# Kernel optimization log

Measured on AMD Instinct MI355X. Metric: run time of the kernel, lower is better.

The kernel has to match this reference:

```python
import jax, jax.numpy as jnp
import numpy as np

B, C, H, W = 4, 256, 64, 64
CH = C // 2  # inner channels of the non-local block


def _conv1x1(x, w, b):
    # 1x1 conv == channel-mixing einsum; x: [B,C,H,W], w: [O,C], b: [O]
    return jnp.einsum('oc,bchw->bohw', w, x) + b[None, :, None, None]


def setup_inputs() -> dict:
    key = jax.random.key(0)
    ks = jax.random.split(key, 9)
    s = 0.02  # small init so exp(scores) stays in fp32 range (no max-subtraction in this block)
    return {
        'x':  jax.random.normal(ks[0], (B, C, H, W), dtype=jnp.float32),
        'w1': s * jax.random.normal(ks[1], (CH, C), dtype=jnp.float32),
        'b1': jnp.zeros((CH,), jnp.float32),
        'w2': s * jax.random.normal(ks[2], (CH, C), dtype=jnp.float32),
        'b2': jnp.zeros((CH,), jnp.float32),
        'w3': s * jax.random.normal(ks[3], (CH, C), dtype=jnp.float32),
        'b3': jnp.zeros((CH,), jnp.float32),
        'w4': s * jax.random.normal(ks[4], (C, CH), dtype=jnp.float32),
        'b4': jnp.zeros((C,), jnp.float32),
    }


def reference(x, w1, b1, w2, b2, w3, b3, w4, b4):
    b, c, h, w = x.shape
    n = h * w
    theta = _conv1x1(x, w1, b1).reshape(b, -1, n)  # [B, C/2, N]
    phi   = _conv1x1(x, w2, b2).reshape(b, -1, n)  # [B, C/2, N]
    g     = _conv1x1(x, w3, b3).reshape(b, -1, n)  # [B, C/2, N]
    # full non-local affinity: [B, N, N]
    scores = jnp.einsum('bci,bcj->bij', theta, phi)
    attn = jnp.exp(scores)  # faithful: no max-subtraction in the original
    attn = attn / jnp.sum(attn, axis=1, keepdims=True)  # normalize over dim=1 as written
    y = jnp.einsum('bij,bcj->bci', attn, g)  # [B, C/2, N]
    y = y.reshape(b, -1, h, w)               # [B, C/2, H, W]
    out = _conv1x1(y, w4, b4) + x            # project back to C, residual
    return out
```

## Files before the change

kernel.cpp:

```cpp
#include <hip/hip_runtime.h>

#define DEVI __device__ __forceinline__

typedef __attribute__((ext_vector_type(8))) short bf16x8;
typedef __attribute__((ext_vector_type(4))) short bf16x4;
typedef __attribute__((ext_vector_type(4))) float f32x4;

#define MFMA16 __builtin_amdgcn_mfma_f32_16x16x32_bf16

DEVI short f2bs(float f) {
  union { float f; unsigned u; } v; v.f = f;
  unsigned r = v.u + 0x7fffu + ((v.u >> 16) & 1u);
  return (short)(r >> 16);
}
DEVI float bs2f(short s) {
  union { unsigned u; float f; } v; v.u = ((unsigned)(unsigned short)s) << 16;
  return v.f;
}

DEVI void gload_lds16(const short* g, short* lds) {
  __builtin_amdgcn_global_load_lds(
      (const __attribute__((address_space(1))) unsigned int*)g,
      (__attribute__((address_space(3))) unsigned int*)lds, 16, 0, 0);
}

DEVI void stage_chunk(short* lds, const short* g, int ldg, int tid) {
#pragma unroll
  for (int it = 0; it < 2; ++it) {
    int slot = it * 256 + tid;
    int row  = slot >> 2;
    int ko   = (slot & 3) << 3;
    gload_lds16(g + (size_t)row * ldg + ko, lds + slot * 8);
  }
}

DEVI void stage_chunk64(short* lds, const short* g, int ldg, int tid) {
  int row = tid >> 2, ko = (tid & 3) << 3;
  gload_lds16(g + (size_t)row * ldg + ko, lds + tid * 8);
}

DEVI bf16x8 lds8(const short* p) { return *(const bf16x8*)p; }

DEVI void zero_acc(f32x4 (&a)[4][4]) {
  f32x4 z = {0.f, 0.f, 0.f, 0.f};
#pragma unroll
  for (int i = 0; i < 4; ++i)
#pragma unroll
    for (int j = 0; j < 4; ++j) a[i][j] = z;
}

__global__ __launch_bounds__(256) void k_prep(const float* __restrict__ x,
                                              const float* __restrict__ w1,
                                              const float* __restrict__ w2,
                                              const float* __restrict__ w3,
                                              short* __restrict__ xt,
                                              short* __restrict__ w123) {
  int tid = threadIdx.x;
  if (blockIdx.y == 4) {
    int lin = blockIdx.z * 64 + blockIdx.x;
    for (int i = lin * 256 + tid; i < 384 * 256; i += 65536) {
      int r = i >> 8;
      const float* w = (r < 128) ? w1 : (r < 256 ? w2 : w3);
      w123[i] = f2bs(w[(size_t)(r & 127) * 256 + (i & 255)]);
    }
    return;
  }
  __shared__ float t[64][65];
  int b = blockIdx.z;
  int c0 = blockIdx.y * 64;
  int p0 = blockIdx.x * 64;
  const float* xb = x + (size_t)b * 256 * 4096;
#pragma unroll
  for (int i = 0; i < 16; ++i) {
    int idx = i * 256 + tid;
    int c = idx >> 6, p = idx & 63;
    t[p][c] = xb[(size_t)(c0 + c) * 4096 + p0 + p];
  }
  __syncthreads();
  short* xtb = xt + ((size_t)b * 4096 + p0) * 256 + c0;
#pragma unroll
  for (int i = 0; i < 16; ++i) {
    int idx = i * 256 + tid;
    int p = idx >> 6, c = idx & 63;
    xtb[(size_t)p * 256 + c] = f2bs(t[p][c]);
  }
}

__global__ __launch_bounds__(256) void k_proj(const short* __restrict__ xt,
                                              const short* __restrict__ w123,
                                              const float* __restrict__ b1,
                                              const float* __restrict__ b2,
                                              const float* __restrict__ b3,
                                              short* __restrict__ theta,
                                              short* __restrict__ phi,
                                              short* __restrict__ gT) {
  __shared__ short Lp[17408];
  int tid = threadIdx.x;
  int m0 = blockIdx.x * 128;
  int nb = blockIdx.y;
  int b  = blockIdx.z;
  int lane = tid & 63, wid = tid >> 6;
  int col = lane & 15, quad = lane >> 4;
  int wm = (wid >> 1) * 64, wn = (wid & 1) * 64;
  const short* A = xt + ((size_t)b * 4096 + m0) * 256;
  const short* B = w123 + (size_t)nb * 128 * 256;
  short* a0 = Lp;           short* b0 = Lp + 4096;
  short* a1 = Lp + 8192;    short* b1_ = Lp + 12288;
  stage_chunk(a0, A, 256, tid);
  stage_chunk(b0, B, 256, tid);
  f32x4 acc[4][4];
  zero_acc(acc);
  for (int ks = 0; ks < 8; ++ks) {
    short* ac = (ks & 1) ? a1 : a0;
    short* an = (ks & 1) ? a0 : a1;
    short* bc = (ks & 1) ? b1_ : b0;
    short* bn = (ks & 1) ? b0 : b1_;
    __syncthreads();
    if (ks < 7) {
      stage_chunk(an, A + (ks + 1) * 32, 256, tid);
      stage_chunk(bn, B + (ks + 1) * 32, 256, tid);
    }
    bf16x8 af[4], bf_[4];
#pragma unroll
    for (int mi = 0; mi < 4; ++mi) af[mi] = lds8(&ac[(wm + mi * 16 + col) * 32 + quad * 8]);
#pragma unroll
    for (int ni = 0; ni < 4; ++ni) bf_[ni] = lds8(&bc[(wn + ni * 16 + col) * 32 + quad * 8]);
#pragma unroll
    for (int mi = 0; mi < 4; ++mi)
#pragma unroll
      for (int ni = 0; ni < 4; ++ni)
        acc[mi][ni] = MFMA16(af[mi], bf_[ni], acc[mi][ni], 0, 0, 0);
  }
  const float* bias = (nb == 0) ? b1 : (nb == 1 ? b2 : b3);
  __syncthreads();
  short* oL = Lp;
  if (nb < 2) {
#pragma unroll
    for (int mi = 0; mi < 4; ++mi)
#pragma unroll
      for (int ni = 0; ni < 4; ++ni) {
        float bv = bias[wn + ni * 16 + col];
#pragma unroll
        for (int r = 0; r < 4; ++r)
          oL[(wm + mi * 16 + quad * 4 + r) * 136 + wn + ni * 16 + col] = f2bs(acc[mi][ni][r] + bv);
      }
    __syncthreads();
    short* O = ((nb == 0) ? theta : phi) + ((size_t)b * 4096 + m0) * 128;
#pragma unroll
    for (int it = 0; it < 8; ++it) {
      int slot = it * 256 + tid;
      int r = slot >> 4, cp = (slot & 15) * 8;
      *(bf16x8*)(O + (size_t)r * 128 + cp) = lds8(&oL[r * 136 + cp]);
    }
  } else {
#pragma unroll
    for (int mi = 0; mi < 4; ++mi)
#pragma unroll
      for (int ni = 0; ni < 4; ++ni) {
        float bv = bias[wn + ni * 16 + col];
#pragma unroll
        for (int r = 0; r < 4; ++r)
          oL[(wn + ni * 16 + col) * 136 + wm + mi * 16 + quad * 4 + r] = f2bs(acc[mi][ni][r] + bv);
      }
    __syncthreads();
    short* O = gT + (size_t)b * 128 * 4096 + m0;
#pragma unroll
    for (int it = 0; it < 8; ++it) {
      int slot = it * 256 + tid;
      int c = slot >> 4, p8 = (slot & 15) * 8;
      *(bf16x8*)(O + (size_t)c * 4096 + p8) = lds8(&oL[c * 136 + p8]);
    }
  }
}

__global__ __launch_bounds__(256, 2) void k_denom(const short* __restrict__ theta,
                                                  const short* __restrict__ phi,
                                                  float* __restrict__ dpart) {
  __shared__ short L[16384];
  __shared__ float part[128];
  int tid = threadIdx.x;
  int ib = blockIdx.x, jc = blockIdx.y, b = blockIdx.z;
  int lane = tid & 63, wid = tid >> 6;
  int col = lane & 15, quad = lane >> 4;
  int wmj = (wid & 1) * 32;
  int wni = (wid >> 1) * 64;
  const short* TH = theta + ((size_t)b * 4096 + ib * 128) * 128;
  const short* PH = phi + ((size_t)b * 4096 + (size_t)jc * 1024) * 128;
  float* D = dpart + ((size_t)(b * 32 + ib)) * 4096 + jc * 1024;
#pragma unroll
  for (int ks = 0; ks < 4; ++ks) stage_chunk(L + ks * 4096, TH + ks * 32, 128, tid);
  __syncthreads();
  bf16x8 bth[4][4];
#pragma unroll
  for (int ks = 0; ks < 4; ++ks)
#pragma unroll
    for (int ni = 0; ni < 4; ++ni)
      bth[ks][ni] = lds8(&L[ks * 4096 + (wni + ni * 16 + col) * 32 + quad * 8]);
  __syncthreads();
#pragma unroll
  for (int ks = 0; ks < 4; ++ks) stage_chunk64(L + ks * 2048, PH + ks * 32, 128, tid);
  for (int jt = 0; jt < 16; ++jt) {
    short* phc = L + (jt & 1) * 8192;
    short* phn = L + ((jt & 1) ^ 1) * 8192;
    __syncthreads();
    if (jt < 15) {
      const short* PHn = PH + (size_t)(jt + 1) * 64 * 128;
#pragma unroll
      for (int ks = 0; ks < 4; ++ks) stage_chunk64(phn + ks * 2048, PHn + ks * 32, 128, tid);
    }
    f32x4 s[2][4];
#pragma unroll
    for (int mi = 0; mi < 2; ++mi)
#pragma unroll
      for (int ni = 0; ni < 4; ++ni) s[mi][ni] = (f32x4){0.f, 0.f, 0.f, 0.f};
#pragma unroll
    for (int ks = 0; ks < 4; ++ks) {
      bf16x8 ap[2];
#pragma unroll
      for (int mi = 0; mi < 2; ++mi) ap[mi] = lds8(&phc[ks * 2048 + (wmj + mi * 16 + col) * 32 + quad * 8]);
#pragma unroll
      for (int mi = 0; mi < 2; ++mi)
#pragma unroll
        for (int ni = 0; ni < 4; ++ni)
          s[mi][ni] = MFMA16(ap[mi], bth[ks][ni], s[mi][ni], 0, 0, 0);
    }
#pragma unroll
    for (int mi = 0; mi < 2; ++mi)
#pragma unroll
      for (int r = 0; r < 4; ++r) {
        float ps = __expf(s[mi][0][r]) + __expf(s[mi][1][r]) +
                   __expf(s[mi][2][r]) + __expf(s[mi][3][r]);
        ps += __shfl_xor(ps, 1, 16);
        ps += __shfl_xor(ps, 2, 16);
        ps += __shfl_xor(ps, 4, 16);
        ps += __shfl_xor(ps, 8, 16);
        if (col == 0) part[(wid >> 1) * 64 + wmj + mi * 16 + quad * 4 + r] = ps;
      }
    __syncthreads();
    if (tid < 64) D[jt * 64 + tid] = part[tid] + part[64 + tid];
  }
}

__global__ __launch_bounds__(256) void k_dred(const float* __restrict__ dpart,
                                              float* __restrict__ dinv) {
  int b = blockIdx.x >> 2, jb = blockIdx.x & 3;
  int j4 = jb * 1024 + threadIdx.x * 4;
  f32x4 s = {0.f, 0.f, 0.f, 0.f};
  for (int ib = 0; ib < 32; ++ib)
    s += *(const f32x4*)(dpart + ((size_t)(b * 32 + ib)) * 4096 + j4);
  f32x4 r;
#pragma unroll
  for (int e = 0; e < 4; ++e) r[e] = 1.0f / s[e];
  *(f32x4*)(dinv + (size_t)b * 4096 + j4) = r;
}

__global__ __launch_bounds__(256, 2) void k_attn(const short* __restrict__ theta,
                                                 const short* __restrict__ phi,
                                                 const short* __restrict__ gT,
                                                 const float* __restrict__ dinv,
                                                 short* __restrict__ ypart) {
  __shared__ short L[40960];
  int tid = threadIdx.x;
  int ib = blockIdx.x, jc = blockIdx.y, b = blockIdx.z;
  int lane = tid & 63, wid = tid >> 6;
  int col = lane & 15, quad = lane >> 4;
  int wmj = (wid & 1) * 32;
  int wni = (wid >> 1) * 64;
  int wnc = (wid & 1) * 64;
  const short* TH = theta + ((size_t)b * 4096 + ib * 128) * 128;
  const short* PH = phi + ((size_t)b * 4096 + (size_t)jc * 1024) * 128;
  const short* GT = gT + (size_t)b * 128 * 4096 + jc * 1024;
  const float* DI = dinv + (size_t)b * 4096 + jc * 1024;
  short* pP = L + 32768;
#pragma unroll
  for (int ks = 0; ks < 4; ++ks) stage_chunk(L + ks * 4096, TH + ks * 32, 128, tid);
  __syncthreads();
  bf16x8 bth[4][4];
#pragma unroll
  for (int ks = 0; ks < 4; ++ks)
#pragma unroll
    for (int ni = 0; ni < 4; ++ni)
      bth[ks][ni] = lds8(&L[ks * 4096 + (wni + ni * 16 + col) * 32 + quad * 8]);
  __syncthreads();
#pragma unroll
  for (int ks = 0; ks < 4; ++ks) stage_chunk64(L + ks * 2048, PH + ks * 32, 128, tid);
#pragma unroll
  for (int s = 0; s < 2; ++s) stage_chunk(L + 16384 + s * 4096, GT + s * 32, 4096, tid);
  f32x4 accy[4][4];
  zero_acc(accy);
  for (int jt = 0; jt < 16; ++jt) {
    int cur = jt & 1;
    short* phc = L + cur * 8192;
    short* phn = L + (cur ^ 1) * 8192;
    short* gpc = L + 16384 + cur * 8192;
    short* gpn = L + 16384 + (cur ^ 1) * 8192;
    __syncthreads();
    if (jt < 15) {
      const short* PHn = PH + (size_t)(jt + 1) * 64 * 128;
#pragma unroll
      for (int ks = 0; ks < 4; ++ks) stage_chunk64(phn + ks * 2048, PHn + ks * 32, 128, tid);
    }
    f32x4 dv[2];
#pragma unroll
    for (int mi = 0; mi < 2; ++mi)
      dv[mi] = *(const f32x4*)(DI + jt * 64 + wmj + mi * 16 + quad * 4);
    f32x4 s[2][4];
#pragma unroll
    for (int mi = 0; mi < 2; ++mi)
#pragma unroll
      for (int ni = 0; ni < 4; ++ni) s[mi][ni] = (f32x4){0.f, 0.f, 0.f, 0.f};
#pragma unroll
    for (int ks = 0; ks < 4; ++ks) {
      bf16x8 ap[2];
#pragma unroll
      for (int mi = 0; mi < 2; ++mi) ap[mi] = lds8(&phc[ks * 2048 + (wmj + mi * 16 + col) * 32 + quad * 8]);
#pragma unroll
      for (int mi = 0; mi < 2; ++mi)
#pragma unroll
        for (int ni = 0; ni < 4; ++ni)
          s[mi][ni] = MFMA16(ap[mi], bth[ks][ni], s[mi][ni], 0, 0, 0);
    }
#pragma unroll
    for (int mi = 0; mi < 2; ++mi) {
      int j0 = wmj + mi * 16 + quad * 4;
      int blk = j0 >> 3, off = j0 & 7;
#pragma unroll
      for (int ni = 0; ni < 4; ++ni) {
        int i = wni + ni * 16 + col;
        bf16x4 pv;
#pragma unroll
        for (int r = 0; r < 4; ++r) pv[r] = f2bs(__expf(s[mi][ni][r]) * dv[mi][r]);
        *(bf16x4*)(pP + i * 64 + ((blk ^ (i & 7)) << 3) + off) = pv;
      }
    }
    __syncthreads();
    if (jt < 15) {
      const short* GTn = GT + (jt + 1) * 64;
#pragma unroll
      for (int s2 = 0; s2 < 2; ++s2) stage_chunk(gpn + s2 * 4096, GTn + s2 * 32, 4096, tid);
    }
#pragma unroll
    for (int ksj = 0; ksj < 2; ++ksj) {
      bf16x8 ap2[4], bg[4];
#pragma unroll
      for (int mi = 0; mi < 4; ++mi) {
        int i = wni + mi * 16 + col;
        ap2[mi] = lds8(&pP[i * 64 + (((ksj * 4 + quad) ^ (i & 7)) << 3)]);
      }
#pragma unroll
      for (int ni = 0; ni < 4; ++ni) bg[ni] = lds8(&gpc[ksj * 4096 + (wnc + ni * 16 + col) * 32 + quad * 8]);
#pragma unroll
      for (int mi = 0; mi < 4; ++mi)
#pragma unroll
        for (int ni = 0; ni < 4; ++ni)
          accy[mi][ni] = MFMA16(ap2[mi], bg[ni], accy[mi][ni], 0, 0, 0);
    }
  }
  short* Yp = ypart + ((size_t)(jc * 4 + b) * 4096 + (size_t)ib * 128) * 128;
#pragma unroll
  for (int half = 0; half < 2; ++half) {
    __syncthreads();
    if ((wid >> 1) == half) {
#pragma unroll
      for (int mi = 0; mi < 4; ++mi)
#pragma unroll
        for (int ni = 0; ni < 4; ++ni)
#pragma unroll
          for (int r = 0; r < 4; ++r)
            pP[(mi * 16 + quad * 4 + r) * 128 + wnc + ni * 16 + col] = f2bs(accy[mi][ni][r]);
    }
    __syncthreads();
#pragma unroll
    for (int it = 0; it < 4; ++it) {
      int slot = it * 256 + tid;
      int r = slot >> 4, c8 = (slot & 15) * 8;
      *(bf16x8*)(Yp + (size_t)(half * 64 + r) * 128 + c8) = lds8(&pP[r * 128 + c8]);
    }
  }
}

__global__ __launch_bounds__(256) void k_out(const short* __restrict__ ypart,
                                             const float* __restrict__ w4,
                                             const float* __restrict__ b4,
                                             const float* __restrict__ x,
                                             float* __restrict__ out) {
  __shared__ short wL[4 * 4096];
  __shared__ short yL[4 * 4096];
  __shared__ float bLs[128];
  int tid = threadIdx.x;
  int ibk = blockIdx.x, ob = blockIdx.y, b = blockIdx.z;
  int o0 = ob * 128, i0 = ibk * 128;
  int lane = tid & 63, wid = tid >> 6;
  int col = lane & 15, quad = lane >> 4;
  int wm = (wid >> 1) * 64, wn = (wid & 1) * 64;
#pragma unroll
  for (int it = 0; it < 16; ++it) {
    int slot = it * 256 + tid;
    int r = slot >> 5, c4 = (slot & 31) * 4;
    int ks = c4 >> 5, cr = c4 & 31;
    f32x4 wv = *(const f32x4*)(w4 + (size_t)(o0 + r) * 128 + c4);
    bf16x4 wp;
#pragma unroll
    for (int e = 0; e < 4; ++e) wp[e] = f2bs(wv[e]);
    *(bf16x4*)&wL[ks * 4096 + r * 32 + cr] = wp;
  }
#pragma unroll
  for (int it = 0; it < 8; ++it) {
    int slot = it * 256 + tid;
    int r = slot >> 4, c8 = (slot & 15) * 8;
    int ks = c8 >> 5, cr = c8 & 31;
    float a8[8];
#pragma unroll
    for (int e = 0; e < 8; ++e) a8[e] = 0.f;
#pragma unroll
    for (int p = 0; p < 4; ++p) {
      bf16x8 v = *(const bf16x8*)(ypart + ((size_t)(p * 4 + b) * 4096 + i0 + r) * 128 + c8);
#pragma unroll
      for (int e = 0; e < 8; ++e) a8[e] += bs2f(v[e]);
    }
    bf16x8 yv;
#pragma unroll
    for (int e = 0; e < 8; ++e) yv[e] = f2bs(a8[e]);
    *(bf16x8*)&yL[ks * 4096 + r * 32 + cr] = yv;
  }
  if (tid < 128) bLs[tid] = b4[o0 + tid];
  __syncthreads();
  f32x4 acc[4][4];
  zero_acc(acc);
#pragma unroll
  for (int ks = 0; ks < 4; ++ks) {
    bf16x8 af[4], bf_[4];
#pragma unroll
    for (int mi = 0; mi < 4; ++mi) af[mi] = lds8(&wL[ks * 4096 + (wm + mi * 16 + col) * 32 + quad * 8]);
#pragma unroll
    for (int ni = 0; ni < 4; ++ni) bf_[ni] = lds8(&yL[ks * 4096 + (wn + ni * 16 + col) * 32 + quad * 8]);
#pragma unroll
    for (int mi = 0; mi < 4; ++mi)
#pragma unroll
      for (int ni = 0; ni < 4; ++ni)
        acc[mi][ni] = MFMA16(af[mi], bf_[ni], acc[mi][ni], 0, 0, 0);
  }
  const float* X = x + ((size_t)b * 256 + o0) * 4096 + i0;
  float* O = out + ((size_t)b * 256 + o0) * 4096 + i0;
#pragma unroll
  for (int mi = 0; mi < 4; ++mi)
#pragma unroll
    for (int ni = 0; ni < 4; ++ni)
#pragma unroll
      for (int r = 0; r < 4; ++r) {
        int o = wm + mi * 16 + quad * 4 + r;
        int i = wn + ni * 16 + col;
        O[(size_t)o * 4096 + i] = acc[mi][ni][r] + X[(size_t)o * 4096 + i] + bLs[o];
      }
}

extern "C" void kernel_launch(void* const* d_in, const int* in_sizes, int n_in,
                              void* d_out, int out_size, void* d_ws, size_t ws_size,
                              hipStream_t stream) {
  const float* x  = (const float*)d_in[0];
  const float* w1 = (const float*)d_in[1];
  const float* b1 = (const float*)d_in[2];
  const float* w2 = (const float*)d_in[3];
  const float* b2 = (const float*)d_in[4];
  const float* w3 = (const float*)d_in[5];
  const float* b3 = (const float*)d_in[6];
  const float* w4 = (const float*)d_in[7];
  const float* b4 = (const float*)d_in[8];
  char* ws = (char*)d_ws;
  short* xt    = (short*)(ws + 0);
  short* w123  = (short*)(ws + 8388608);
  short* theta = (short*)(ws + 8585216);
  short* phi   = (short*)(ws + 12779520);
  short* gT    = (short*)(ws + 16973824);
  float* dpart = (float*)(ws + 21168128);
  float* dinv  = (float*)(ws + 23265280);
  short* ypart = (short*)(ws + 23330816);
  float* out   = (float*)d_out;
  (void)in_sizes; (void)n_in; (void)out_size; (void)ws_size;

  k_prep<<<dim3(64, 5, 4), dim3(256), 0, stream>>>(x, w1, w2, w3, xt, w123);
  k_proj<<<dim3(32, 3, 4), dim3(256), 0, stream>>>(xt, w123, b1, b2, b3, theta, phi, gT);
  k_denom<<<dim3(32, 4, 4), dim3(256), 0, stream>>>(theta, phi, dpart);
  k_dred<<<dim3(16), dim3(256), 0, stream>>>(dpart, dinv);
  k_attn<<<dim3(32, 4, 4), dim3(256), 0, stream>>>(theta, phi, gT, dinv, ypart);
  k_out<<<dim3(32, 2, 4), dim3(256), 0, stream>>>(ypart, w4, b4, x, out);
}
```

Measured before the change: 187.7 us.

## Fuse bf16 prep into projection and merge attention barriers with lgkm waits

Removes the separate transpose/convert kernel. The projection GEMM now reads fp32 x and weights straight from global memory and converts them to bf16 in registers, with no LDS staging. In the attention kernel, the next gT chunk is prefetched together with phi at the top of each tile, which drops one __syncthreads per iteration. The denominator and attention kernels also replace __syncthreads with a waitcnt on LDS only plus s_barrier. The risks are uncoalesced strided global loads of x in the projection (each lane reads 8 values spaced 4096 floats apart) and a possible race, because the barrier no longer waits on outstanding vmcnt for the global-to-LDS loads.

```diff
diff --git a/kernel.cpp b/kernel.cpp
--- a/kernel.cpp
+++ b/kernel.cpp
@@ -16,6 +16,11 @@
 DEVI float bs2f(short s) {
   union { unsigned u; float f; } v; v.u = ((unsigned)(unsigned short)s) << 16;
   return v.f;
+}
+
+DEVI void lgkm_barrier() {
+  __builtin_amdgcn_s_waitcnt(0xC07F);
+  __builtin_amdgcn_s_barrier();
 }
 
 DEVI void gload_lds16(const short* g, short* lds) {
@@ -49,52 +54,17 @@
     for (int j = 0; j < 4; ++j) a[i][j] = z;
 }
 
-__global__ __launch_bounds__(256) void k_prep(const float* __restrict__ x,
-                                              const float* __restrict__ w1,
-                                              const float* __restrict__ w2,
-                                              const float* __restrict__ w3,
-                                              short* __restrict__ xt,
-                                              short* __restrict__ w123) {
-  int tid = threadIdx.x;
-  if (blockIdx.y == 4) {
-    int lin = blockIdx.z * 64 + blockIdx.x;
-    for (int i = lin * 256 + tid; i < 384 * 256; i += 65536) {
-      int r = i >> 8;
-      const float* w = (r < 128) ? w1 : (r < 256 ? w2 : w3);
-      w123[i] = f2bs(w[(size_t)(r & 127) * 256 + (i & 255)]);
-    }
-    return;
-  }
-  __shared__ float t[64][65];
-  int b = blockIdx.z;
-  int c0 = blockIdx.y * 64;
-  int p0 = blockIdx.x * 64;
-  const float* xb = x + (size_t)b * 256 * 4096;
-#pragma unroll
-  for (int i = 0; i < 16; ++i) {
-    int idx = i * 256 + tid;
-    int c = idx >> 6, p = idx & 63;
-    t[p][c] = xb[(size_t)(c0 + c) * 4096 + p0 + p];
-  }
-  __syncthreads();
-  short* xtb = xt + ((size_t)b * 4096 + p0) * 256 + c0;
-#pragma unroll
-  for (int i = 0; i < 16; ++i) {
-    int idx = i * 256 + tid;
-    int p = idx >> 6, c = idx & 63;
-    xtb[(size_t)p * 256 + c] = f2bs(t[p][c]);
-  }
-}
-
-__global__ __launch_bounds__(256) void k_proj(const short* __restrict__ xt,
-                                              const short* __restrict__ w123,
-                                              const float* __restrict__ b1,
-                                              const float* __restrict__ b2,
-                                              const float* __restrict__ b3,
-                                              short* __restrict__ theta,
-                                              short* __restrict__ phi,
-                                              short* __restrict__ gT) {
-  __shared__ short Lp[17408];
+__global__ __launch_bounds__(256, 4) void k_proj(const float* __restrict__ x,
+                                                 const float* __restrict__ w1,
+                                                 const float* __restrict__ w2,
+                                                 const float* __restrict__ w3,
+                                                 const float* __restrict__ b1,
+                                                 const float* __restrict__ b2,
+                                                 const float* __restrict__ b3,
+                                                 short* __restrict__ theta,
+                                                 short* __restrict__ phi,
+                                                 short* __restrict__ gT) {
+  __shared__ short oL[128 * 136];
   int tid = threadIdx.x;
   int m0 = blockIdx.x * 128;
   int nb = blockIdx.y;
@@ -102,29 +72,29 @@
   int lane = tid & 63, wid = tid >> 6;
   int col = lane & 15, quad = lane >> 4;
   int wm = (wid >> 1) * 64, wn = (wid & 1) * 64;
-  const short* A = xt + ((size_t)b * 4096 + m0) * 256;
-  const short* B = w123 + (size_t)nb * 128 * 256;
-  short* a0 = Lp;           short* b0 = Lp + 4096;
-  short* a1 = Lp + 8192;    short* b1_ = Lp + 12288;
-  stage_chunk(a0, A, 256, tid);
-  stage_chunk(b0, B, 256, tid);
+  const float* W = (nb == 0) ? w1 : (nb == 1 ? w2 : w3);
+  const float* X = x + (size_t)b * 256 * 4096;
   f32x4 acc[4][4];
   zero_acc(acc);
+#pragma unroll
   for (int ks = 0; ks < 8; ++ks) {
-    short* ac = (ks & 1) ? a1 : a0;
-    short* an = (ks & 1) ? a0 : a1;
-    short* bc = (ks & 1) ? b1_ : b0;
-    short* bn = (ks & 1) ? b0 : b1_;
-    __syncthreads();
-    if (ks < 7) {
-      stage_chunk(an, A + (ks + 1) * 32, 256, tid);
-      stage_chunk(bn, B + (ks + 1) * 32, 256, tid);
-    }
     bf16x8 af[4], bf_[4];
 #pragma unroll
-    for (int mi = 0; mi < 4; ++mi) af[mi] = lds8(&ac[(wm + mi * 16 + col) * 32 + quad * 8]);
-#pragma unroll
-    for (int ni = 0; ni < 4; ++ni) bf_[ni] = lds8(&bc[(wn + ni * 16 + col) * 32 + quad * 8]);
+    for (int mi = 0; mi < 4; ++mi) {
+      int pix = m0 + wm + mi * 16 + col;
+      const float* xp = X + (size_t)(ks * 32 + quad * 8) * 4096 + pix;
+#pragma unroll
+      for (int e = 0; e < 8; ++e) af[mi][e] = f2bs(xp[(size_t)e * 4096]);
+    }
+#pragma unroll
+    for (int ni = 0; ni < 4; ++ni) {
+      int o = wn + ni * 16 + col;
+      const float* wp = W + (size_t)o * 256 + ks * 32 + quad * 8;
+      f32x4 wv0 = *(const f32x4*)wp;
+      f32x4 wv1 = *(const f32x4*)(wp + 4);
+#pragma unroll
+      for (int e = 0; e < 4; ++e) { bf_[ni][e] = f2bs(wv0[e]); bf_[ni][4 + e] = f2bs(wv1[e]); }
+    }
 #pragma unroll
     for (int mi = 0; mi < 4; ++mi)
 #pragma unroll
@@ -132,8 +102,6 @@
         acc[mi][ni] = MFMA16(af[mi], bf_[ni], acc[mi][ni], 0, 0, 0);
   }
   const float* bias = (nb == 0) ? b1 : (nb == 1 ? b2 : b3);
-  __syncthreads();
-  short* oL = Lp;
   if (nb < 2) {
 #pragma unroll
     for (int mi = 0; mi < 4; ++mi)
@@ -236,7 +204,7 @@
         ps += __shfl_xor(ps, 8, 16);
         if (col == 0) part[(wid >> 1) * 64 + wmj + mi * 16 + quad * 4 + r] = ps;
       }
-    __syncthreads();
+    lgkm_barrier();
     if (tid < 64) D[jt * 64 + tid] = part[tid] + part[64 + tid];
   }
 }
@@ -295,15 +263,18 @@
     short* gpc = L + 16384 + cur * 8192;
     short* gpn = L + 16384 + (cur ^ 1) * 8192;
     __syncthreads();
+    f32x4 dv[2];
+#pragma unroll
+    for (int mi = 0; mi < 2; ++mi)
+      dv[mi] = *(const f32x4*)(DI + jt * 64 + wmj + mi * 16 + quad * 4);
     if (jt < 15) {
       const short* PHn = PH + (size_t)(jt + 1) * 64 * 128;
 #pragma unroll
       for (int ks = 0; ks < 4; ++ks) stage_chunk64(phn + ks * 2048, PHn + ks * 32, 128, tid);
-    }
-    f32x4 dv[2];
-#pragma unroll
-    for (int mi = 0; mi < 2; ++mi)
-      dv[mi] = *(const f32x4*)(DI + jt * 64 + wmj + mi * 16 + quad * 4);
+      const short* GTn = GT + (jt + 1) * 64;
+#pragma unroll
+      for (int s2 = 0; s2 < 2; ++s2) stage_chunk(gpn + s2 * 4096, GTn + s2 * 32, 4096, tid);
+    }
     f32x4 s[2][4];
 #pragma unroll
     for (int mi = 0; mi < 2; ++mi)
@@ -333,12 +304,7 @@
         *(bf16x4*)(pP + i * 64 + ((blk ^ (i & 7)) << 3) + off) = pv;
       }
     }
-    __syncthreads();
-    if (jt < 15) {
-      const short* GTn = GT + (jt + 1) * 64;
-#pragma unroll
-      for (int s2 = 0; s2 < 2; ++s2) stage_chunk(gpn + s2 * 4096, GTn + s2 * 32, 4096, tid);
-    }
+    lgkm_barrier();
 #pragma unroll
     for (int ksj = 0; ksj < 2; ++ksj) {
       bf16x8 ap2[4], bg[4];
@@ -467,19 +433,16 @@
   const float* w4 = (const float*)d_in[7];
   const float* b4 = (const float*)d_in[8];
   char* ws = (char*)d_ws;
-  short* xt    = (short*)(ws + 0);
-  short* w123  = (short*)(ws + 8388608);
-  short* theta = (short*)(ws + 8585216);
-  short* phi   = (short*)(ws + 12779520);
-  short* gT    = (short*)(ws + 16973824);
-  float* dpart = (float*)(ws + 21168128);
-  float* dinv  = (float*)(ws + 23265280);
-  short* ypart = (short*)(ws + 23330816);
+  short* theta = (short*)(ws + 0);
+  short* phi   = (short*)(ws + 4194304);
+  short* gT    = (short*)(ws + 8388608);
+  float* dpart = (float*)(ws + 12582912);
+  float* dinv  = (float*)(ws + 14680064);
+  short* ypart = (short*)(ws + 14745600);
   float* out   = (float*)d_out;
   (void)in_sizes; (void)n_in; (void)out_size; (void)ws_size;
 
-  k_prep<<<dim3(64, 5, 4), dim3(256), 0, stream>>>(x, w1, w2, w3, xt, w123);
-  k_proj<<<dim3(32, 3, 4), dim3(256), 0, stream>>>(xt, w123, b1, b2, b3, theta, phi, gT);
+  k_proj<<<dim3(32, 3, 4), dim3(256), 0, stream>>>(x, w1, w2, w3, b1, b2, b3, theta, phi, gT);
   k_denom<<<dim3(32, 4, 4), dim3(256), 0, stream>>>(theta, phi, dpart);
   k_dred<<<dim3(16), dim3(256), 0, stream>>>(dpart, dinv);
   k_attn<<<dim3(32, 4, 4), dim3(256), 0, stream>>>(theta, phi, gT, dinv, ypart);
```

New measurement: 210.9 us. 12.4% more time.
